# Kernel optimization log

Hardware: AMD Instinct MI355X
Metric: run time of the kernel (lower is better)

The kernel has to match this reference:

```python
import jax, jax.numpy as jnp
import numpy as np

B, T, C, H = 8, 2048, 1024, 64  # batch, seq_len(block_size), embedding_size, head_size


def setup_inputs() -> dict:
    key = jax.random.key(0)
    kx, kk, kq, kv = jax.random.split(key, 4)
    x = jax.random.normal(kx, (B, T, C), dtype=jnp.float32)
    # nn.Linear(C, H, bias=False) weights, stored as [in, out] for x @ W
    s = 1.0 / np.sqrt(C)
    Wk = jax.random.uniform(kk, (C, H), dtype=jnp.float32, minval=-s, maxval=s)
    Wq = jax.random.uniform(kq, (C, H), dtype=jnp.float32, minval=-s, maxval=s)
    Wv = jax.random.uniform(kv, (C, H), dtype=jnp.float32, minval=-s, maxval=s)
    return {"x": x, "Wk": Wk, "Wq": Wq, "Wv": Wv}


def reference(x, Wk, Wq, Wv):
    Bx, Tx, Cx = x.shape
    k = jnp.einsum('btc,ch->bth', x, Wk)
    q = jnp.einsum('btc,ch->bth', x, Wq)
    v = jnp.einsum('btc,ch->bth', x, Wv)
    # NOTE: original scales by embedding dim C ** -0.5, not head_size
    scores = jnp.einsum('bth,bsh->bts', q, k) * (Cx ** -0.5)  # [B,T,T]
    causal = jnp.tril(jnp.ones((Tx, Tx), dtype=bool))
    scores = jnp.where(causal, scores, -jnp.inf)
    attn = jax.nn.softmax(scores, axis=-1)
    # dropout is identity in eval/deterministic mode
    out = jnp.einsum('bts,bsh->bth', attn, v)  # [B,T,H]
    return out
```

## Files before the change

### kernel.cpp

```cpp
#include <hip/hip_runtime.h>
#include <hip/hip_bf16.h>
#include <math.h>


#define BT 16384
#define TSEQ 2048
#define XST 72

typedef __attribute__((ext_vector_type(8))) __bf16 bf16x8;
typedef __attribute__((ext_vector_type(8))) unsigned short ushort8;
typedef __attribute__((ext_vector_type(4))) float floatx4;

#define MFMA16(a, b, c) __builtin_amdgcn_mfma_f32_16x16x32_bf16( \
    __builtin_bit_cast(bf16x8, (a)), __builtin_bit_cast(bf16x8, (b)), (c), 0, 0, 0)

__device__ inline unsigned short f2bf(float f) {
  unsigned u = __builtin_bit_cast(unsigned, f);
  u += 0x7FFFu + ((u >> 16) & 1u);
  return (unsigned short)(u >> 16);
}
__device__ inline float bf2f(unsigned short s) {
  return __builtin_bit_cast(float, (unsigned)s << 16);
}
__device__ inline unsigned long long pack4bf(floatx4 f) {
  return (unsigned long long)f2bf(f[0]) | ((unsigned long long)f2bf(f[1]) << 16) |
         ((unsigned long long)f2bf(f[2]) << 32) | ((unsigned long long)f2bf(f[3]) << 48);
}
__device__ inline ushort8 pack8bf(floatx4 a, floatx4 b) {
  ushort8 t;
#pragma unroll
  for (int i = 0; i < 4; ++i) t[i] = f2bf(a[i]);
#pragma unroll
  for (int i = 0; i < 4; ++i) t[4 + i] = f2bf(b[i]);
  return t;
}
__device__ inline void glds16(const unsigned short* g, unsigned short* l) {
  __builtin_amdgcn_global_load_lds(
      (const __attribute__((address_space(1))) unsigned int*)g,
      (__attribute__((address_space(3))) unsigned int*)l, 16, 0, 0);
}

__global__ __launch_bounds__(256) void wt2_kernel(
    const float* __restrict__ Wq, const float* __restrict__ Wk,
    const float* __restrict__ Wv, unsigned short* __restrict__ Wt2) {
  __shared__ float ls[64][65];
  const int m = blockIdx.x >> 4;
  const int kci = blockIdx.x & 15;
  const int c0 = kci << 6;
  const float* __restrict__ W = (m == 0) ? Wq : (m == 1) ? Wk : Wv;
  const int tid = threadIdx.x;
#pragma unroll
  for (int i = 0; i < 16; ++i) {
    int idx = tid + (i << 8);
    int cl = idx >> 6, h = idx & 63;
    ls[cl][h] = W[(c0 + cl) * 64 + h];
  }
  __syncthreads();
  const int w = tid >> 6, lane = tid & 63;
  const int quad = lane >> 4, l16 = lane & 15;
  const int nt = (m << 2) + w;
#pragma unroll
  for (int half = 0; half < 2; ++half) {
    ushort8 t;
#pragma unroll
    for (int j = 0; j < 8; ++j)
      t[j] = f2bf(ls[(half << 5) + (quad << 3) + j][(w << 4) + l16]);
    *(ushort8*)(Wt2 + ((size_t)(((nt << 4) + kci) * 2 + half) << 9) +
                (lane << 3)) = t;
  }
}

#define XBS 4608
#define BB0 9216
#define BBS 12288

__global__ __launch_bounds__(512) void qkv_mfma(
    const float* __restrict__ x, const unsigned short* __restrict__ Wt2,
    unsigned short* __restrict__ Qf, unsigned short* __restrict__ Kf,
    unsigned short* __restrict__ Vf) {
  __shared__ __align__(16) unsigned short smem[46080];

  const int tid = threadIdx.x;
  const int w = tid >> 6, lane = tid & 63;
  const int quad = lane >> 4, l16 = lane & 15;
  const int wr = w >> 2, wn = w & 3;
  const int r0 = blockIdx.x << 6;
  const int xrow = (w << 3) + (lane >> 3);
  const int xcol = (lane & 7) << 3;
  const float* __restrict__ xp = x + (size_t)(r0 + xrow) * 1024 + xcol;
  const int xw_u16 = xrow * XST + xcol;

  floatx4 acc[2][3];
#pragma unroll
  for (int rt = 0; rt < 2; ++rt)
#pragma unroll
    for (int n = 0; n < 3; ++n) acc[rt][n] = (floatx4){0.f, 0.f, 0.f, 0.f};

  floatx4 pf[4][2];

#pragma unroll
  for (int i = 0; i < 3; ++i) {
    const int f = 3 * w + i;
    glds16(Wt2 + ((size_t)(((f >> 1) << 4) * 2 + (f & 1)) << 9) + (lane << 3),
           &smem[BB0 + (f << 9)]);
  }
  __builtin_amdgcn_sched_barrier(0);
#pragma unroll
  for (int s = 0; s < 4; ++s) {
    pf[s][0] = *(const floatx4*)(xp + (s << 6));
    pf[s][1] = *(const floatx4*)(xp + (s << 6) + 4);
  }
  __builtin_amdgcn_sched_barrier(0);
#pragma unroll
  for (int i = 0; i < 3; ++i) {
    const int f = 3 * w + i;
    glds16(Wt2 + ((size_t)((((f >> 1) << 4) + 1) * 2 + (f & 1)) << 9) +
               (lane << 3),
           &smem[BB0 + BBS + (f << 9)]);
  }
  __builtin_amdgcn_sched_barrier(0);
  *(ushort8*)&smem[xw_u16] = pack8bf(pf[0][0], pf[0][1]);
  __builtin_amdgcn_sched_barrier(0);
  asm volatile("s_waitcnt vmcnt(11)");
  asm volatile("s_waitcnt lgkmcnt(0)");
  __builtin_amdgcn_sched_barrier(0);
  __builtin_amdgcn_s_barrier();
  __builtin_amdgcn_sched_barrier(0);

#pragma unroll
  for (int c = 0; c < 16; ++c) {
    if (c + 1 < 16)
      *(ushort8*)&smem[((c + 1) & 1) * XBS + xw_u16] =
          pack8bf(pf[(c + 1) & 3][0], pf[(c + 1) & 3][1]);
    __builtin_amdgcn_sched_barrier(0);
    if (c + 2 < 16) {
#pragma unroll
      for (int i = 0; i < 3; ++i) {
        const int f = 3 * w + i;
        glds16(Wt2 + ((size_t)((((f >> 1) << 4) + (c + 2)) * 2 + (f & 1)) << 9) +
                   (lane << 3),
               &smem[BB0 + ((c + 2) % 3) * BBS + (f << 9)]);
      }
    }
    __builtin_amdgcn_sched_barrier(0);
    if (c + 4 < 16) {
      pf[c & 3][0] = *(const floatx4*)(xp + ((c + 4) << 6));
      pf[c & 3][1] = *(const floatx4*)(xp + ((c + 4) << 6) + 4);
    }
    __builtin_amdgcn_sched_barrier(0);

    ushort8 af[2][2];
#pragma unroll
    for (int rt = 0; rt < 2; ++rt)
#pragma unroll
      for (int h = 0; h < 2; ++h)
        af[rt][h] = *(const ushort8*)&smem[(c & 1) * XBS +
            ((wr << 5) + (rt << 4) + l16) * XST + (h << 5) + (quad << 3)];
    ushort8 bfr[3][2];
#pragma unroll
    for (int n = 0; n < 3; ++n)
#pragma unroll
      for (int h = 0; h < 2; ++h)
        bfr[n][h] = *(const ushort8*)&smem[BB0 + (c % 3) * BBS +
            ((((3 * wn + n) << 1) + h) << 9) + (lane << 3)];
#pragma unroll
    for (int h = 0; h < 2; ++h)
#pragma unroll
      for (int rt = 0; rt < 2; ++rt)
#pragma unroll
        for (int n = 0; n < 3; ++n)
          acc[rt][n] = MFMA16(af[rt][h], bfr[n][h], acc[rt][n]);

    __builtin_amdgcn_sched_barrier(0);
    if (c <= 11)      { asm volatile("s_waitcnt vmcnt(7)"); }
    else if (c == 12) { asm volatile("s_waitcnt vmcnt(5)"); }
    else if (c == 13) { asm volatile("s_waitcnt vmcnt(3)"); }
    else              { asm volatile("s_waitcnt vmcnt(0)"); }
    asm volatile("s_waitcnt lgkmcnt(0)");
    __builtin_amdgcn_sched_barrier(0);
    __builtin_amdgcn_s_barrier();
    __builtin_amdgcn_sched_barrier(0);
  }

#pragma unroll
  for (int n = 0; n < 3; ++n) {
    const int nt = 3 * wn + n;
    const int m = nt >> 2, hg = nt & 3;
#pragma unroll
    for (int rt = 0; rt < 2; ++rt) {
      const int rowb = (wr << 5) + (rt << 4) + (quad << 2);
      if (m < 2) {
#pragma unroll
        for (int r = 0; r < 4; ++r)
          smem[m * XBS + (rowb + r) * XST + (hg << 4) + l16] =
              f2bf(acc[rt][n][r]);
      } else {
        *(unsigned long long*)&smem[2 * XBS + ((hg << 4) + l16) * XST + rowb] =
            pack4bf(acc[rt][n]);
      }
    }
  }
  __syncthreads();

  const int b = blockIdx.x >> 5, st = blockIdx.x & 31;
#pragma unroll
  for (int i = 0; i < 3; ++i) {
    const int f = w * 3 + i;
    const int m = f >> 3, idx = f & 7, grp = idx >> 1, kh = idx & 1;
    ushort8 t = *(const ushort8*)&smem[m * XBS + ((grp << 4) + l16) * XST +
                                       (kh << 5) + (quad << 3)];
    unsigned short* dst;
    if (m == 0)
      dst = Qf + (((size_t)(b * 128 + (st << 2) + grp) * 2 + kh) << 9);
    else if (m == 1)
      dst = Kf + (((size_t)((b * 32 + st) * 4 + grp) * 2 + kh) << 9);
    else
      dst = Vf + (((size_t)((b * 32 + st) * 4 + grp) * 2 + kh) << 9);
    *(ushort8*)(dst + (lane << 3)) = t;
  }
}

__global__ __launch_bounds__(256, 3) void attn_part(
    const unsigned short* __restrict__ Qf, const unsigned short* __restrict__ Kf,
    const unsigned short* __restrict__ Vf, float* __restrict__ part) {
  __shared__ __align__(16) unsigned short KV[2][8192];
  __shared__ unsigned short Pw[4][16 * XST];

  const int tid = threadIdx.x;
  const int w = tid >> 6, lane = tid & 63;
  const int quad = lane >> 4, l16 = lane & 15;
  const int b = blockIdx.x / 144;
  const int e = blockIdx.x - b * 144;
  int g = 0;
#pragma unroll
  for (int gg = 1; gg < 8; ++gg) g += (e >= 2 * gg * (gg + 1)) ? 1 : 0;
  const int rem2 = e - 2 * g * (g + 1);
  const int qt = (g << 2) + rem2 / (g + 1);
  const int ch = rem2 - (rem2 / (g + 1)) * (g + 1);
  const int s0 = ch << 2;
  const int s1 = (s0 + 4 < qt + 1) ? s0 + 4 : qt + 1;
  const int r16 = (qt << 2) + w;

#define KVIDX(ss, nt, kh) \
  (((((size_t)(b * 32 + (ss)) << 2) + (nt)) * 2 + (kh)) << 9)
#define STAGE_KV(ss, db)                                                     \
  {                                                                          \
    _Pragma("unroll") for (int r_ = 0; r_ < 4; ++r_) {                       \
      const int f_ = (r_ << 2) + w;                                          \
      const unsigned short* src_ =                                           \
          (f_ < 8) ? Kf + KVIDX(ss, (f_ >> 1), (f_ & 1)) + (lane << 3)       \
                   : Vf + KVIDX(ss, (f_ >> 1) - 4, (f_ & 1)) + (lane << 3);  \
      glds16(src_, &KV[db][f_ << 9]);                                        \
    }                                                                        \
  }

  const unsigned short* qbase =
      Qf + ((((size_t)b * 128 + r16) * 2) << 9) + (lane << 3);
  ushort8 qf0 = *(const ushort8*)qbase;
  ushort8 qf1 = *(const ushort8*)(qbase + 512);
  __builtin_amdgcn_sched_barrier(0);

  STAGE_KV(s0, 0);
  __builtin_amdgcn_sched_barrier(0);
  STAGE_KV((s0 + 1 < s1) ? s0 + 1 : s1 - 1, 1);
  __builtin_amdgcn_sched_barrier(0);
  asm volatile("s_waitcnt vmcnt(4)");
  __builtin_amdgcn_sched_barrier(0);
  __builtin_amdgcn_s_barrier();
  __builtin_amdgcn_sched_barrier(0);

  floatx4 acc[4], lacc;
#pragma unroll
  for (int nt = 0; nt < 4; ++nt) acc[nt] = (floatx4){0.f, 0.f, 0.f, 0.f};
  lacc = (floatx4){0.f, 0.f, 0.f, 0.f};
  const ushort8 ones = {0x3F80, 0x3F80, 0x3F80, 0x3F80,
                        0x3F80, 0x3F80, 0x3F80, 0x3F80};

  for (int s = s0; s < s1; ++s) {
    const int cur = (s - s0) & 1;
    ushort8 bk[4][2], bv[4][2];
#pragma unroll
    for (int nt = 0; nt < 4; ++nt)
#pragma unroll
      for (int kh = 0; kh < 2; ++kh) {
        bk[nt][kh] = *(const ushort8*)&KV[cur][((((nt << 1) + kh)) << 9) +
                                              (lane << 3)];
        bv[nt][kh] = *(const ushort8*)&KV[cur][(((8 + (nt << 1) + kh)) << 9) +
                                              (lane << 3)];
      }
    asm volatile("s_waitcnt lgkmcnt(0)");
    __builtin_amdgcn_sched_barrier(0);
    __builtin_amdgcn_s_barrier();
    __builtin_amdgcn_sched_barrier(0);

    STAGE_KV((s + 2 < s1) ? s + 2 : s1 - 1, cur);
    __builtin_amdgcn_sched_barrier(0);

    floatx4 sf[4];
#pragma unroll
    for (int nt = 0; nt < 4; ++nt) {
      sf[nt] = (floatx4){0.f, 0.f, 0.f, 0.f};
      sf[nt] = MFMA16(qf0, bk[nt][0], sf[nt]);
      sf[nt] = MFMA16(qf1, bk[nt][1], sf[nt]);
    }

    const bool diag = (s == qt);
    const int qrow = (w << 4) + (quad << 2);
#pragma unroll
    for (int nt = 0; nt < 4; ++nt) {
      const int keyl = (nt << 4) + l16;
#pragma unroll
      for (int r = 0; r < 4; ++r) {
        float ev = __expf(sf[nt][r] * 0.03125f);
        if (diag && keyl > qrow + r) ev = 0.f;
        Pw[w][((quad << 2) + r) * XST + keyl] = f2bf(ev);
      }
    }

#pragma unroll
    for (int kh = 0; kh < 2; ++kh) {
      ushort8 pa = *(const ushort8*)&Pw[w][l16 * XST + (kh << 5) + (quad << 3)];
      lacc = MFMA16(pa, ones, lacc);
#pragma unroll
      for (int nt = 0; nt < 4; ++nt) acc[nt] = MFMA16(pa, bv[nt][kh], acc[nt]);
    }

    __builtin_amdgcn_sched_barrier(0);
    asm volatile("s_waitcnt vmcnt(4)");
    __builtin_amdgcn_sched_barrier(0);
    __builtin_amdgcn_s_barrier();
    __builtin_amdgcn_sched_barrier(0);
  }
#undef STAGE_KV
#undef KVIDX

  float* slot = part + (size_t)(b * 144 + e) * 2112;
  if (l16 == 0) {
#pragma unroll
    for (int r = 0; r < 4; ++r) slot[(w << 4) + (quad << 2) + r] = lacc[r];
  }
  unsigned short* op = (unsigned short*)(slot + 64);
#pragma unroll
  for (int nt = 0; nt < 4; ++nt)
#pragma unroll
    for (int r = 0; r < 4; ++r)
      op[((w << 4) + (quad << 2) + r) * 64 + (nt << 4) + l16] = f2bf(acc[nt][r]);
}

__global__ __launch_bounds__(256) void attn_combine(
    const float* __restrict__ part, float* __restrict__ out) {
  const int rh = blockIdx.x & 1;
  const int bqt = blockIdx.x >> 1;
  const int b = bqt >> 5, qt = bqt & 31;
  const int tid = threadIdx.x;
  const int row = (rh << 5) + (tid >> 3);
  const int hseg = (tid & 7) << 3;
  const int g = qt >> 2;
  const int nch = g + 1;
  const int ebase = 2 * g * (g + 1) + (qt & 3) * (g + 1);

  float l = 0.f;
  float ov[8];
#pragma unroll
  for (int i = 0; i < 8; ++i) ov[i] = 0.f;
  for (int c = 0; c < nch; ++c) {
    const float* slot = part + (size_t)(b * 144 + ebase + c) * 2112;
    l += slot[row];
    ushort8 o0 = *(const ushort8*)((const unsigned short*)(slot + 64) +
                                   row * 64 + hseg);
#pragma unroll
    for (int i = 0; i < 8; ++i) ov[i] += bf2f(o0[i]);
  }
  const float inv = 1.f / l;
  float* o = out + ((size_t)(b * TSEQ + (qt << 6) + row)) * 64 + hseg;
#pragma unroll
  for (int i = 0; i < 8; ++i) o[i] = ov[i] * inv;
}

extern "C" void kernel_launch(void* const* d_in, const int* in_sizes, int n_in,
                              void* d_out, int out_size, void* d_ws, size_t ws_size,
                              hipStream_t stream) {
  const float* x  = (const float*)d_in[0];
  const float* Wk = (const float*)d_in[1];
  const float* Wq = (const float*)d_in[2];
  const float* Wv = (const float*)d_in[3];

  unsigned short* Qfw = (unsigned short*)d_ws;
  unsigned short* Kfw = Qfw + (size_t)BT * 64;
  unsigned short* Vfw = Kfw + (size_t)BT * 64;
  unsigned short* Wt2 = Vfw + (size_t)BT * 64;
  float* part = (float*)(Wt2 + 3 * 64 * 1024);

  wt2_kernel<<<48, 256, 0, stream>>>(Wq, Wk, Wv, Wt2);
  qkv_mfma<<<256, 512, 0, stream>>>(x, Wt2, Qfw, Kfw, Vfw);
  attn_part<<<1152, 256, 0, stream>>>(Qfw, Kfw, Vfw, part);
  attn_combine<<<512, 256, 0, stream>>>(part, (float*)d_out);
}
```

Measured before the change: 129.3 us.

## Fuse split-K combine into attention kernel via last-block atomic counter

Removes the separate attn_combine launch. Each attn_part block increments a per-(batch, q-tile) atomic counter, and the last block to finish reduces the partial results and writes the output. Tiles with a single chunk write the normalized output directly and skip the partial buffer. The counters are zeroed in wt2_kernel. This saves one kernel launch and the partial-buffer round trip for single-chunk tiles, at the cost of atomics, extra syncthreads, and serial combine work in the tail blocks.

Measured after the change: 171.4 us. 1.33x slower.

```diff
diff --git a/kernel.cpp b/kernel.cpp
--- a/kernel.cpp
+++ b/kernel.cpp
@@ -42,13 +42,15 @@
 
 __global__ __launch_bounds__(256) void wt2_kernel(
     const float* __restrict__ Wq, const float* __restrict__ Wk,
-    const float* __restrict__ Wv, unsigned short* __restrict__ Wt2) {
+    const float* __restrict__ Wv, unsigned short* __restrict__ Wt2,
+    int* __restrict__ cnt) {
   __shared__ float ls[64][65];
   const int m = blockIdx.x >> 4;
   const int kci = blockIdx.x & 15;
   const int c0 = kci << 6;
   const float* __restrict__ W = (m == 0) ? Wq : (m == 1) ? Wk : Wv;
   const int tid = threadIdx.x;
+  if (blockIdx.x == 0) cnt[tid] = 0;
 #pragma unroll
   for (int i = 0; i < 16; ++i) {
     int idx = tid + (i << 8);
@@ -222,9 +224,11 @@
 
 __global__ __launch_bounds__(256, 3) void attn_part(
     const unsigned short* __restrict__ Qf, const unsigned short* __restrict__ Kf,
-    const unsigned short* __restrict__ Vf, float* __restrict__ part) {
+    const unsigned short* __restrict__ Vf, float* __restrict__ part,
+    int* __restrict__ cnt, float* __restrict__ out) {
   __shared__ __align__(16) unsigned short KV[2][8192];
   __shared__ unsigned short Pw[4][16 * XST];
+  __shared__ int lastFlag;
 
   const int tid = threadIdx.x;
   const int w = tid >> 6, lane = tid & 63;
@@ -240,6 +244,7 @@
   const int s0 = ch << 2;
   const int s1 = (s0 + 4 < qt + 1) ? s0 + 4 : qt + 1;
   const int r16 = (qt << 2) + w;
+  const int nch = g + 1;
 
 #define KVIDX(ss, nt, kh) \
   (((((size_t)(b * 32 + (ss)) << 2) + (nt)) * 2 + (kh)) << 9)
@@ -334,6 +339,18 @@
 #undef STAGE_KV
 #undef KVIDX
 
+  if (nch == 1) {
+#pragma unroll
+    for (int r = 0; r < 4; ++r) {
+      const float inv = 1.f / lacc[r];
+      const int row = (qt << 6) + (w << 4) + (quad << 2) + r;
+      float* o = out + ((size_t)(b * TSEQ + row)) * 64 + l16;
+#pragma unroll
+      for (int nt = 0; nt < 4; ++nt) o[nt << 4] = acc[nt][r] * inv;
+    }
+    return;
+  }
+
   float* slot = part + (size_t)(b * 144 + e) * 2112;
   if (l16 == 0) {
 #pragma unroll
@@ -345,36 +362,38 @@
 #pragma unroll
     for (int r = 0; r < 4; ++r)
       op[((w << 4) + (quad << 2) + r) * 64 + (nt << 4) + l16] = f2bf(acc[nt][r]);
-}
-
-__global__ __launch_bounds__(256) void attn_combine(
-    const float* __restrict__ part, float* __restrict__ out) {
-  const int rh = blockIdx.x & 1;
-  const int bqt = blockIdx.x >> 1;
-  const int b = bqt >> 5, qt = bqt & 31;
-  const int tid = threadIdx.x;
-  const int row = (rh << 5) + (tid >> 3);
-  const int hseg = (tid & 7) << 3;
-  const int g = qt >> 2;
-  const int nch = g + 1;
-  const int ebase = 2 * g * (g + 1) + (qt & 3) * (g + 1);
-
-  float l = 0.f;
-  float ov[8];
-#pragma unroll
-  for (int i = 0; i < 8; ++i) ov[i] = 0.f;
-  for (int c = 0; c < nch; ++c) {
-    const float* slot = part + (size_t)(b * 144 + ebase + c) * 2112;
-    l += slot[row];
-    ushort8 o0 = *(const ushort8*)((const unsigned short*)(slot + 64) +
-                                   row * 64 + hseg);
-#pragma unroll
-    for (int i = 0; i < 8; ++i) ov[i] += bf2f(o0[i]);
-  }
-  const float inv = 1.f / l;
-  float* o = out + ((size_t)(b * TSEQ + (qt << 6) + row)) * 64 + hseg;
-#pragma unroll
-  for (int i = 0; i < 8; ++i) o[i] = ov[i] * inv;
+
+  __syncthreads();
+  if (tid == 0) {
+    int old = __hip_atomic_fetch_add(&cnt[(b << 5) + qt], 1, __ATOMIC_ACQ_REL,
+                                     __HIP_MEMORY_SCOPE_AGENT);
+    lastFlag = (old == nch - 1);
+  }
+  __syncthreads();
+  if (!lastFlag) return;
+
+  const int ebase = e - ch;
+#pragma unroll
+  for (int rh = 0; rh < 2; ++rh) {
+    const int row = (rh << 5) + (tid >> 3);
+    const int hseg = (tid & 7) << 3;
+    float l = 0.f;
+    float ov[8];
+#pragma unroll
+    for (int i = 0; i < 8; ++i) ov[i] = 0.f;
+    for (int c2 = 0; c2 < nch; ++c2) {
+      const float* s2 = part + (size_t)(b * 144 + ebase + c2) * 2112;
+      l += s2[row];
+      ushort8 o0 = *(const ushort8*)((const unsigned short*)(s2 + 64) +
+                                     row * 64 + hseg);
+#pragma unroll
+      for (int i = 0; i < 8; ++i) ov[i] += bf2f(o0[i]);
+    }
+    const float inv = 1.f / l;
+    float* o = out + ((size_t)(b * TSEQ + (qt << 6) + row)) * 64 + hseg;
+#pragma unroll
+    for (int i = 0; i < 8; ++i) o[i] = ov[i] * inv;
+  }
 }
 
 extern "C" void kernel_launch(void* const* d_in, const int* in_sizes, int n_in,
@@ -390,9 +409,9 @@
   unsigned short* Vfw = Kfw + (size_t)BT * 64;
   unsigned short* Wt2 = Vfw + (size_t)BT * 64;
   float* part = (float*)(Wt2 + 3 * 64 * 1024);
-
-  wt2_kernel<<<48, 256, 0, stream>>>(Wq, Wk, Wv, Wt2);
+  int* cnt = (int*)(part + (size_t)1152 * 2112);
+
+  wt2_kernel<<<48, 256, 0, stream>>>(Wq, Wk, Wv, Wt2, cnt);
   qkv_mfma<<<256, 512, 0, stream>>>(x, Wt2, Qfw, Kfw, Vfw);
-  attn_part<<<1152, 256, 0, stream>>>(Qfw, Kfw, Vfw, part);
-  attn_combine<<<512, 256, 0, stream>>>(part, (float*)d_out);
-}
+  attn_part<<<1152, 256, 0, stream>>>(Qfw, Kfw, Vfw, part, cnt, (float*)d_out);
+}
```
